# Performance work log

Measured on AMD Instinct MI355X. Metric: run time of the kernel, lower is better.

## Reference

```python
import jax, jax.numpy as jnp
import numpy as np

R = 4          # num_roles
L = 2          # num_layers
DIN = 128      # input/hidden feature dim
DOUT = 40     # output classes
N = 40000      # nodes
E = 480000     # edges


def setup_inputs() -> dict:
    key = jax.random.key(0)
    ks = jax.random.split(key, 12)
    x = jax.random.normal(ks[0], (N, R + DIN), dtype=jnp.float32)
    edge_index = jax.random.randint(ks[1], (2, E), 0, N, dtype=jnp.int64)
    s = 0.05
    Wm = jax.random.normal(ks[2], (L, R, DIN, DIN), dtype=jnp.float32) * s
    bm = jax.random.normal(ks[3], (L, R, DIN), dtype=jnp.float32) * s
    Wa = jax.random.normal(ks[4], (L, R, 2 * DIN, DIN), dtype=jnp.float32) * s
    ba = jax.random.normal(ks[5], (L, R, DIN), dtype=jnp.float32) * s
    W1 = jax.random.normal(ks[6], (DIN, DIN), dtype=jnp.float32) * s
    b1 = jax.random.normal(ks[7], (DIN,), dtype=jnp.float32) * s
    W2 = jax.random.normal(ks[8], (DIN, DOUT), dtype=jnp.float32) * s
    b2 = jax.random.normal(ks[9], (DOUT,), dtype=jnp.float32) * s
    return {"x": x, "edge_index": edge_index, "Wm": Wm, "bm": bm,
            "Wa": Wa, "ba": ba, "W1": W1, "b1": b1, "W2": W2, "b2": b2}


def _role_coef(roles):
    # Faithful to the original loop bug: linears[0] applied twice with roles[:,0],
    # linears[r] with roles[:,r] for r=1..R-2, linears[R-1] unused.
    return jnp.concatenate(
        [2.0 * roles[:, :1], roles[:, 1:R - 1], jnp.zeros_like(roles[:, :1])], axis=1)


def _graphsage_layer(xfull, src, dst, Wm_l, bm_l, Wa_l, ba_l):
    roles = xfull[:, :R]          # [N, R]
    feats = xfull[:, R:]          # [N, D]
    # --- message: gather source nodes, per-role linear + weighted sum, relu ---
    xr = roles[src]               # [E, R]
    xf = feats[src]               # [E, D]
    coef = _role_coef(xr)         # [E, R]
    lin = jnp.einsum('ei,rio->ero', xf, Wm_l) + bm_l[None]   # [E, R, O]
    msg = jax.nn.relu(jnp.einsum('er,ero->eo', coef, lin))    # [E, O]
    # --- aggregate: scatter-mean to target nodes ---
    ssum = jax.ops.segment_sum(msg, dst, num_segments=N)      # [N, O]
    cnt = jax.ops.segment_sum(jnp.ones((msg.shape[0], 1), msg.dtype), dst,
                              num_segments=N)                 # [N, 1]
    aggr = jnp.where(cnt > 0, ssum / jnp.maximum(cnt, 1.0), 0.0)
    # --- update: concat, per-role linear + weighted sum, relu, L2 normalize ---
    cat = jnp.concatenate([feats, aggr], axis=1)              # [N, D+O]
    coefn = _role_coef(roles)                                 # [N, R]
    lin2 = jnp.einsum('ni,rio->nro', cat, Wa_l) + ba_l[None]  # [N, R, O]
    out = jax.nn.relu(jnp.einsum('nr,nro->no', coefn, lin2))  # [N, O]
    norm = jnp.linalg.norm(out, axis=1, keepdims=True)
    return out / jnp.maximum(norm, 1e-12)


def reference(x, edge_index, Wm, bm, Wa, ba, W1, b1, W2, b2):
    src = edge_index[0]
    dst = edge_index[1]
    h = x
    for l in range(L):
        feats = _graphsage_layer(h, src, dst, Wm[l], bm[l], Wa[l], ba[l])
        feats = jax.nn.relu(feats)  # extra relu from GNNStack (dropout is identity in eval)
        h = jnp.concatenate([h[:, :R], feats], axis=1)
    z = h[:, R:]
    z = z @ W1 + b1               # post_mp linear 1 (dropout identity)
    logits = z @ W2 + b2          # post_mp linear 2
    return jax.nn.log_softmax(logits, axis=1)
```

## Files before the change

### kernel.cpp

```cpp
#include <hip/hip_runtime.h>
#include <hip/hip_fp16.h>

#define RN 4
#define XSTRIDE 132

typedef float    frag_cd __attribute__((ext_vector_type(4)));
typedef _Float16 frag_h  __attribute__((ext_vector_type(8)));

#define CW_M  (6 * 128 * 128)
#define CW_A  (6 * 128 * 256)
#define CW_1  (128 * 128)
#define CW_2  (48 * 128)
#define CW_TOT (CW_M + CW_A + CW_1 + CW_2)

__global__ void prep_kernel(
    const float* __restrict__ Wm, const float* __restrict__ Wa,
    const float* __restrict__ W1, const float* __restrict__ W2,
    _Float16* __restrict__ WmT, _Float16* __restrict__ WaT,
    _Float16* __restrict__ W1T, _Float16* __restrict__ W2T,
    const float* __restrict__ x, _Float16* __restrict__ X,
    const int* __restrict__ ei, int* __restrict__ cnt, int N, int E)
{
    int id = blockIdx.x * 256 + threadIdx.x;
    if (id < CW_M) {
        const int K = 128;
        int per = K * 128;
        int lr = id / per;  int l = lr / 3, r = lr - l * 3;
        int rem = id - lr * per;
        int k = rem >> 7, col = rem & 127;
        WmT[((size_t)lr * 128 + col) * K + k] =
            (_Float16)Wm[(((size_t)l * 4 + r) * K + k) * 128 + col];
        return;
    }
    id -= CW_M;
    if (id < CW_A) {
        const int K = 256;
        int per = K * 128;
        int lr = id / per;  int l = lr / 3, r = lr - l * 3;
        int rem = id - lr * per;
        int k = rem >> 7, col = rem & 127;
        WaT[((size_t)lr * 128 + col) * K + k] =
            (_Float16)Wa[(((size_t)l * 4 + r) * K + k) * 128 + col];
        return;
    }
    id -= CW_A;
    if (id < CW_1) {
        int col = id >> 7, k = id & 127;
        W1T[id] = (_Float16)W1[k * 128 + col];
        return;
    }
    id -= CW_1;
    if (id < CW_2) {
        int col = id >> 7, k = id & 127;
        W2T[id] = (_Float16)((col < 40) ? W2[k * 40 + col] : 0.0f);
        return;
    }
    id -= CW_2;
    if (id < N * 16) {
        int n = id >> 4, g = id & 15;
        const float4* src = (const float4*)(x + (size_t)n * XSTRIDE + RN + g * 8);
        float4 f0 = src[0], f1 = src[1];
        __half2 h0 = __float22half2_rn(make_float2(f0.x, f0.y));
        __half2 h1 = __float22half2_rn(make_float2(f0.z, f0.w));
        __half2 h2 = __float22half2_rn(make_float2(f1.x, f1.y));
        __half2 h3 = __float22half2_rn(make_float2(f1.z, f1.w));
        uint4 st; st.x = *(uint*)&h0; st.y = *(uint*)&h1;
        st.z = *(uint*)&h2; st.w = *(uint*)&h3;
        ((uint4*)X)[(size_t)n * 16 + g] = st;
        return;
    }
    id -= N * 16;
    if (id < E) atomicAdd(&cnt[ei[E + id]], 1);
}

__global__ void scanA(const int* __restrict__ cnt, int N, int* __restrict__ bsums) {
    __shared__ int s[256];
    int t = threadIdx.x, n = blockIdx.x * 256 + t;
    s[t] = (n < N) ? cnt[n] : 0;
    __syncthreads();
    for (int off = 128; off > 0; off >>= 1) {
        if (t < off) s[t] += s[t + off];
        __syncthreads();
    }
    if (t == 0) bsums[blockIdx.x] = s[0];
}

__global__ void scanC(const int* __restrict__ cnt, int N, int nb,
                      const int* __restrict__ bsums, int* __restrict__ offs) {
    __shared__ int s[256];
    __shared__ int basebuf[256];
    int t = threadIdx.x, n = blockIdx.x * 256 + t;
    int bid = blockIdx.x;
    basebuf[t] = (t < bid && t < nb) ? bsums[t] : 0;
    __syncthreads();
    for (int off = 128; off > 0; off >>= 1) {
        if (t < off) basebuf[t] += basebuf[t + off];
        __syncthreads();
    }
    int base = basebuf[0];
    int v = (n < N) ? cnt[n] : 0;
    s[t] = v; __syncthreads();
    for (int off = 1; off < 256; off <<= 1) {
        int add = (t >= off) ? s[t - off] : 0;
        __syncthreads();
        s[t] += add;
        __syncthreads();
    }
    if (n < N) {
        offs[n] = base + s[t] - v;
        if (n == N - 1) offs[N] = base + s[t];
    }
}

__global__ void fill_kernel(const int* __restrict__ ei, int E,
                            const int* __restrict__ offs, int* __restrict__ fc,
                            int* __restrict__ csr) {
    int e = blockIdx.x * 256 + threadIdx.x;
    if (e < E) {
        int dst = ei[E + e];
        int p = offs[dst] + atomicAdd(&fc[dst], 1);
        csr[p] = ei[e];
    }
}

__global__ __launch_bounds__(256) void agg_kernel(
    const int* __restrict__ csr, const int* __restrict__ offs,
    const _Float16* __restrict__ Mb, _Float16* __restrict__ S, int N)
{
    int node = blockIdx.x * 16 + (threadIdx.x >> 4);
    int lane = threadIdx.x & 15;
    if (node >= N) return;
    int lo = offs[node], hi = offs[node + 1];
    const uint4* M4 = (const uint4*)Mb;
    float a[8];
    #pragma unroll
    for (int i = 0; i < 8; ++i) a[i] = 0.0f;
    int e = lo;
    for (; e + 3 < hi; e += 4) {
        #pragma unroll
        for (int j = 0; j < 4; ++j) {
            uint4 u = M4[(size_t)csr[e + j] * 16 + lane];
            float2 f0 = __half22float2(*(const __half2*)&u.x);
            float2 f1 = __half22float2(*(const __half2*)&u.y);
            float2 f2 = __half22float2(*(const __half2*)&u.z);
            float2 f3 = __half22float2(*(const __half2*)&u.w);
            a[0] += f0.x; a[1] += f0.y; a[2] += f1.x; a[3] += f1.y;
            a[4] += f2.x; a[5] += f2.y; a[6] += f3.x; a[7] += f3.y;
        }
    }
    for (; e < hi; ++e) {
        uint4 u = M4[(size_t)csr[e] * 16 + lane];
        float2 f0 = __half22float2(*(const __half2*)&u.x);
        float2 f1 = __half22float2(*(const __half2*)&u.y);
        float2 f2 = __half22float2(*(const __half2*)&u.z);
        float2 f3 = __half22float2(*(const __half2*)&u.w);
        a[0] += f0.x; a[1] += f0.y; a[2] += f1.x; a[3] += f1.y;
        a[4] += f2.x; a[5] += f2.y; a[6] += f3.x; a[7] += f3.y;
    }
    float inv = (hi > lo) ? 1.0f / (float)(hi - lo) : 0.0f;
    __half2 h0 = __float22half2_rn(make_float2(a[0] * inv, a[1] * inv));
    __half2 h1 = __float22half2_rn(make_float2(a[2] * inv, a[3] * inv));
    __half2 h2 = __float22half2_rn(make_float2(a[4] * inv, a[5] * inv));
    __half2 h3 = __float22half2_rn(make_float2(a[6] * inv, a[7] * inv));
    uint4 st; st.x = *(uint*)&h0; st.y = *(uint*)&h1;
    st.z = *(uint*)&h2; st.w = *(uint*)&h3;
    ((uint4*)S)[(size_t)node * 16 + lane] = st;
}

#define STAGE_TILE(dst, src, n0, tid)                                         \
    _Pragma("unroll")                                                         \
    for (int i_ = 0; i_ < 4; ++i_) {                                          \
        int idx_ = i_ * 256 + (tid);                                          \
        int row_ = idx_ >> 4, g_ = idx_ & 15;                                 \
        *(uint4*)&(dst)[row_][g_ * 8] =                                       \
            ((const uint4*)(src))[((size_t)((n0) + row_)) * 16 + g_];         \
    }

__global__ __launch_bounds__(256) void msg_kernel(
    const float* __restrict__ x,
    const _Float16* __restrict__ Fp,
    const _Float16* __restrict__ W,
    const float* __restrict__ bias,
    _Float16* __restrict__ out)
{
    __shared__ _Float16 As[64][136];
    __shared__ float cc[64][3];

    const int tid = threadIdx.x;
    const int n0 = blockIdx.x * 64;
    const int lane = tid & 63;
    const int wv = tid >> 6;
    const int q = lane >> 4;
    const int lb = lane & 15;
    const int w32 = wv * 32;

    if (tid < 64) {
        const float* xr = x + (size_t)(n0 + tid) * XSTRIDE;
        cc[tid][0] = 2.0f * xr[0];
        cc[tid][1] = xr[1];
        cc[tid][2] = xr[2];
    }
    STAGE_TILE(As, Fp, n0, tid)
    __syncthreads();

    _Float16 ch16[4][3];
    #pragma unroll
    for (int nt = 0; nt < 4; ++nt)
        #pragma unroll
        for (int r = 0; r < 3; ++r)
            ch16[nt][r] = (_Float16)cc[nt * 16 + lb][r];

    frag_cd acc[4][2];
    #pragma unroll
    for (int nt = 0; nt < 4; ++nt)
        #pragma unroll
        for (int ct = 0; ct < 2; ++ct)
            acc[nt][ct] = (frag_cd){0.f, 0.f, 0.f, 0.f};

    frag_h bF[4][6];
    #pragma unroll
    for (int c = 0; c < 4; ++c)
        #pragma unroll
        for (int r = 0; r < 3; ++r)
            #pragma unroll
            for (int ct = 0; ct < 2; ++ct)
                bF[c][r * 2 + ct] = *(const frag_h*)(
                    W + ((size_t)(r * 128 + w32 + ct * 16 + lb)) * 128 + c * 32 + q * 8);

    frag_h aL[2][4];
    #pragma unroll
    for (int nt = 0; nt < 4; ++nt)
        aL[0][nt] = *(const frag_h*)&As[nt * 16 + lb][q * 8];

    #pragma unroll
    for (int c = 0; c < 4; ++c) {
        if (c + 1 < 4) {
            #pragma unroll
            for (int nt = 0; nt < 4; ++nt)
                aL[(c + 1) & 1][nt] = *(const frag_h*)&As[nt * 16 + lb][(c + 1) * 32 + q * 8];
        }
        #pragma unroll
        for (int r = 0; r < 3; ++r)
            #pragma unroll
            for (int nt = 0; nt < 4; ++nt) {
                frag_h sa = aL[c & 1][nt] * ch16[nt][r];
                #pragma unroll
                for (int ct = 0; ct < 2; ++ct)
                    acc[nt][ct] = __builtin_amdgcn_mfma_f32_16x16x32_f16(
                        sa, bF[c][r * 2 + ct], acc[nt][ct], 0, 0, 0);
            }
    }

    #pragma unroll
    for (int ct = 0; ct < 2; ++ct) {
        int col = w32 + ct * 16 + lb;
        float b0 = bias[col], b1 = bias[128 + col], b2 = bias[256 + col];
        #pragma unroll
        for (int nt = 0; nt < 4; ++nt)
            #pragma unroll
            for (int rg = 0; rg < 4; ++rg) {
                int row = nt * 16 + q * 4 + rg;
                float v = acc[nt][ct][rg]
                        + cc[row][0] * b0 + cc[row][1] * b1 + cc[row][2] * b2;
                out[(size_t)(n0 + row) * 128 + col] = (_Float16)fmaxf(v, 0.0f);
            }
    }
}

#define UPDATE_PHASE_A_LDS(Wa_, ba_)                                          \
    _Float16 ch16[4][3];                                                      \
    _Pragma("unroll")                                                         \
    for (int nt = 0; nt < 4; ++nt)                                            \
        _Pragma("unroll")                                                     \
        for (int r = 0; r < 3; ++r)                                           \
            ch16[nt][r] = (_Float16)cc[nt * 16 + lb][r];                      \
    frag_cd acc[4][2];                                                        \
    _Pragma("unroll")                                                         \
    for (int nt = 0; nt < 4; ++nt)                                            \
        _Pragma("unroll")                                                     \
        for (int ct = 0; ct < 2; ++ct)                                        \
            acc[nt][ct] = (frag_cd){0.f, 0.f, 0.f, 0.f};                      \
    size_t wrow[3][2];                                                        \
    _Pragma("unroll")                                                         \
    for (int r = 0; r < 3; ++r)                                               \
        _Pragma("unroll")                                                     \
        for (int ct = 0; ct < 2; ++ct)                                        \
            wrow[r][ct] = ((size_t)(r * 128 + w32 + ct * 16 + lb)) * 256 + q * 8; \
    {                                                                         \
        frag_h bF[3][6];                                                      \
        auto loadB = [&](int c, int buf) {                                    \
            _Pragma("unroll")                                                 \
            for (int r = 0; r < 3; ++r)                                       \
                _Pragma("unroll")                                             \
                for (int ct = 0; ct < 2; ++ct)                                \
                    bF[buf][r * 2 + ct] = *(const frag_h*)((Wa_) + wrow[r][ct] + c * 32); \
        };                                                                    \
        loadB(0, 0);                                                          \
        loadB(1, 1);                                                          \
        frag_h aL[2][4];                                                      \
        _Pragma("unroll")                                                     \
        for (int nt = 0; nt < 4; ++nt)                                        \
            aL[0][nt] = *(const frag_h*)&As[nt * 16 + lb][q * 8];             \
        _Pragma("unroll")                                                     \
        for (int ch = 0; ch < 8; ++ch) {                                      \
            if (ch + 2 < 8) loadB(ch + 2, (ch + 2) % 3);                      \
            if (ch + 1 < 8) {                                                 \
                const int c1 = ch + 1;                                        \
                _Pragma("unroll")                                             \
                for (int nt = 0; nt < 4; ++nt)                                \
                    aL[c1 & 1][nt] = (c1 < 4)                                 \
                        ? *(const frag_h*)&As[nt * 16 + lb][c1 * 32 + q * 8]  \
                        : *(const frag_h*)&Ss[nt * 16 + lb][(c1 - 4) * 32 + q * 8]; \
            }                                                                 \
            const int cur = ch % 3;                                           \
            _Pragma("unroll")                                                 \
            for (int r = 0; r < 3; ++r)                                       \
                _Pragma("unroll")                                             \
                for (int nt = 0; nt < 4; ++nt) {                              \
                    frag_h sa = aL[ch & 1][nt] * ch16[nt][r];                 \
                    _Pragma("unroll")                                         \
                    for (int ct = 0; ct < 2; ++ct)                            \
                        acc[nt][ct] = __builtin_amdgcn_mfma_f32_16x16x32_f16( \
                            sa, bF[cur][r * 2 + ct], acc[nt][ct], 0, 0, 0);   \
                }                                                             \
        }                                                                     \
    }                                                                         \
    float vv[4][2][4];                                                        \
    _Pragma("unroll")                                                         \
    for (int ct = 0; ct < 2; ++ct) {                                          \
        int col = w32 + ct * 16 + lb;                                         \
        float b0 = (ba_)[col], b1 = (ba_)[128 + col], b2 = (ba_)[256 + col];  \
        _Pragma("unroll")                                                     \
        for (int nt = 0; nt < 4; ++nt)                                        \
            _Pragma("unroll")                                                 \
            for (int rg = 0; rg < 4; ++rg) {                                  \
                int row = nt * 16 + q * 4 + rg;                               \
                float v = acc[nt][ct][rg]                                     \
                        + cc[row][0] * b0 + cc[row][1] * b1 + cc[row][2] * b2;\
                vv[nt][ct][rg] = fmaxf(v, 0.0f);                              \
            }                                                                 \
    }                                                                         \
    _Pragma("unroll")                                                         \
    for (int nt = 0; nt < 4; ++nt)                                            \
        _Pragma("unroll")                                                     \
        for (int rg = 0; rg < 4; ++rg) {                                      \
            float ss = vv[nt][0][rg] * vv[nt][0][rg] + vv[nt][1][rg] * vv[nt][1][rg]; \
            _Pragma("unroll")                                                 \
            for (int m = 1; m < 16; m <<= 1) ss += __shfl_xor(ss, m, 64);     \
            if (lb == 0) red[nt * 16 + q * 4 + rg][wv] = ss;                  \
        }                                                                     \
    __syncthreads();        \
    _Pragma("unroll")                                                         \
    for (int nt = 0; nt < 4; ++nt)                                            \
        _Pragma("unroll")                                                     \
        for (int rg = 0; rg < 4; ++rg) {                                      \
            int row = nt * 16 + q * 4 + rg;                                   \
            float t = red[row][0] + red[row][1] + red[row][2] + red[row][3];  \
            float inv = 1.0f / fmaxf(sqrtf(t), 1e-12f);                       \
            _Pragma("unroll")                                                 \
            for (int ct = 0; ct < 2; ++ct)                                    \
                Fs[row][w32 + ct * 16 + lb] = (_Float16)(vv[nt][ct][rg] * inv); \
        }                                                                     \
    __syncthreads();

__global__ __launch_bounds__(256) void fused_upd_msg(
    const float* __restrict__ x,
    const _Float16* __restrict__ Fp, const _Float16* __restrict__ Sp,
    const _Float16* __restrict__ Wa_, const float* __restrict__ ba_,
    const _Float16* __restrict__ Wm2, const float* __restrict__ bm2,
    _Float16* __restrict__ F1, _Float16* __restrict__ Mb)
{
    __shared__ _Float16 ldsbuf[2 * 64 * 136];
    __shared__ float cc[64][3];
    __shared__ float red[64][4];
    _Float16 (*As)[136] = (_Float16(*)[136])ldsbuf;
    _Float16 (*Ss)[136] = (_Float16(*)[136])(ldsbuf + 64 * 136);
    _Float16 (*Fs)[136] = As;

    const int tid = threadIdx.x;
    const int n0 = blockIdx.x * 64;
    const int lane = tid & 63;
    const int wv = tid >> 6;
    const int q = lane >> 4;
    const int lb = lane & 15;
    const int w32 = wv * 32;

    if (tid < 64) {
        const float* xr = x + (size_t)(n0 + tid) * XSTRIDE;
        cc[tid][0] = 2.0f * xr[0];
        cc[tid][1] = xr[1];
        cc[tid][2] = xr[2];
    }
    STAGE_TILE(As, Fp, n0, tid)
    STAGE_TILE(Ss, Sp, n0, tid)
    __syncthreads();

    UPDATE_PHASE_A_LDS(Wa_, ba_)

    #pragma unroll
    for (int i = 0; i < 4; ++i) {
        int idx = i * 256 + tid;
        int row = idx >> 4, g = idx & 15;
        ((uint4*)F1)[(size_t)(n0 + row) * 16 + g] = *(const uint4*)&Fs[row][g * 8];
    }

    frag_cd a2[4][2];
    #pragma unroll
    for (int nt = 0; nt < 4; ++nt)
        #pragma unroll
        for (int ct = 0; ct < 2; ++ct)
            a2[nt][ct] = (frag_cd){0.f, 0.f, 0.f, 0.f};

    frag_h bB[4][6];
    #pragma unroll
    for (int c = 0; c < 4; ++c)
        #pragma unroll
        for (int r = 0; r < 3; ++r)
            #pragma unroll
            for (int ct = 0; ct < 2; ++ct)
                bB[c][r * 2 + ct] = *(const frag_h*)(
                    Wm2 + ((size_t)(r * 128 + w32 + ct * 16 + lb)) * 128 + c * 32 + q * 8);

    #pragma unroll
    for (int c = 0; c < 4; ++c) {
        frag_h aM[4];
        #pragma unroll
        for (int nt = 0; nt < 4; ++nt)
            aM[nt] = *(const frag_h*)&Fs[nt * 16 + lb][c * 32 + q * 8];
        #pragma unroll
        for (int r = 0; r < 3; ++r)
            #pragma unroll
            for (int nt = 0; nt < 4; ++nt) {
                frag_h sa = aM[nt] * ch16[nt][r];
                #pragma unroll
                for (int ct = 0; ct < 2; ++ct)
                    a2[nt][ct] = __builtin_amdgcn_mfma_f32_16x16x32_f16(
                        sa, bB[c][r * 2 + ct], a2[nt][ct], 0, 0, 0);
            }
    }

    #pragma unroll
    for (int ct = 0; ct < 2; ++ct) {
        int col = w32 + ct * 16 + lb;
        float b0 = bm2[col], b1 = bm2[128 + col], b2 = bm2[256 + col];
        #pragma unroll
        for (int nt = 0; nt < 4; ++nt)
            #pragma unroll
            for (int rg = 0; rg < 4; ++rg) {
                int row = nt * 16 + q * 4 + rg;
                float v = a2[nt][ct][rg]
                        + cc[row][0] * b0 + cc[row][1] * b1 + cc[row][2] * b2;
                Mb[(size_t)(n0 + row) * 128 + col] = (_Float16)fmaxf(v, 0.0f);
            }
    }
}

__global__ __launch_bounds__(256) void fused_upd_final(
    const float* __restrict__ x,
    const _Float16* __restrict__ Fp, const _Float16* __restrict__ Sp,
    const _Float16* __restrict__ Wa_, const float* __restrict__ ba_,
    const _Float16* __restrict__ W1T, const float* __restrict__ b1,
    const _Float16* __restrict__ W2T, const float* __restrict__ b2,
    float* __restrict__ out)
{
    __shared__ _Float16 ldsbuf[2 * 64 * 136];
    __shared__ float cc[64][3];
    __shared__ float red[64][4];
    _Float16 (*As)[136] = (_Float16(*)[136])ldsbuf;
    _Float16 (*Ss)[136] = (_Float16(*)[136])(ldsbuf + 64 * 136);
    _Float16 (*Fs)[136] = As;
    _Float16 (*Z)[136]  = Ss;

    const int tid = threadIdx.x;
    const int n0 = blockIdx.x * 64;
    const int lane = tid & 63;
    const int wv = tid >> 6;
    const int q = lane >> 4;
    const int lb = lane & 15;
    const int w32 = wv * 32;

    if (tid < 64) {
        const float* xr = x + (size_t)(n0 + tid) * XSTRIDE;
        cc[tid][0] = 2.0f * xr[0];
        cc[tid][1] = xr[1];
        cc[tid][2] = xr[2];
    }
    STAGE_TILE(As, Fp, n0, tid)
    STAGE_TILE(Ss, Sp, n0, tid)
    __syncthreads();

    UPDATE_PHASE_A_LDS(Wa_, ba_)

    frag_cd az[4][2];
    #pragma unroll
    for (int nt = 0; nt < 4; ++nt)
        #pragma unroll
        for (int ct = 0; ct < 2; ++ct)
            az[nt][ct] = (frag_cd){0.f, 0.f, 0.f, 0.f};

    frag_h bZ[4][2];
    #pragma unroll
    for (int c = 0; c < 4; ++c)
        #pragma unroll
        for (int ct = 0; ct < 2; ++ct)
            bZ[c][ct] = *(const frag_h*)(
                W1T + (size_t)(w32 + ct * 16 + lb) * 128 + c * 32 + q * 8);

    #pragma unroll
    for (int c = 0; c < 4; ++c) {
        frag_h aZ[4];
        #pragma unroll
        for (int nt = 0; nt < 4; ++nt)
            aZ[nt] = *(const frag_h*)&Fs[nt * 16 + lb][c * 32 + q * 8];
        #pragma unroll
        for (int ct = 0; ct < 2; ++ct)
            #pragma unroll
            for (int nt = 0; nt < 4; ++nt)
                az[nt][ct] = __builtin_amdgcn_mfma_f32_16x16x32_f16(
                    aZ[nt], bZ[c][ct], az[nt][ct], 0, 0, 0);
    }
    __syncthreads();
    #pragma unroll
    for (int ct = 0; ct < 2; ++ct) {
        int col = w32 + ct * 16 + lb;
        float bb = b1[col];
        #pragma unroll
        for (int nt = 0; nt < 4; ++nt)
            #pragma unroll
            for (int rg = 0; rg < 4; ++rg)
                Z[nt * 16 + q * 4 + rg][col] = (_Float16)(az[nt][ct][rg] + bb);
    }
    __syncthreads();

    frag_cd a2[3];
    #pragma unroll
    for (int ct = 0; ct < 3; ++ct) a2[ct] = (frag_cd){0.f, 0.f, 0.f, 0.f};
    #pragma unroll
    for (int ch = 0; ch < 4; ++ch) {
        frag_h zF = *(const frag_h*)&Z[wv * 16 + lb][ch * 32 + q * 8];
        #pragma unroll
        for (int ct = 0; ct < 3; ++ct) {
            frag_h bF = *(const frag_h*)(W2T + (size_t)(ct * 16 + lb) * 128 + ch * 32 + q * 8);
            a2[ct] = __builtin_amdgcn_mfma_f32_16x16x32_f16(zF, bF, a2[ct], 0, 0, 0);
        }
    }

    float lg[3][4];
    #pragma unroll
    for (int ct = 0; ct < 3; ++ct) {
        int col = ct * 16 + lb;
        bool valid = col < 40;
        float bb = valid ? b2[col] : -1e30f;
        #pragma unroll
        for (int rg = 0; rg < 4; ++rg)
            lg[ct][rg] = valid ? (a2[ct][rg] + bb) : -1e30f;
    }
    #pragma unroll
    for (int rg = 0; rg < 4; ++rg) {
        float mx = fmaxf(fmaxf(lg[0][rg], lg[1][rg]), lg[2][rg]);
        #pragma unroll
        for (int m = 1; m < 16; m <<= 1) mx = fmaxf(mx, __shfl_xor(mx, m, 64));
        float sm = __expf(lg[0][rg] - mx) + __expf(lg[1][rg] - mx) + __expf(lg[2][rg] - mx);
        #pragma unroll
        for (int m = 1; m < 16; m <<= 1) sm += __shfl_xor(sm, m, 64);
        float ls = mx + __logf(sm);
        int row = n0 + wv * 16 + q * 4 + rg;
        #pragma unroll
        for (int ct = 0; ct < 3; ++ct) {
            int col = ct * 16 + lb;
            if (col < 40) out[(size_t)row * 40 + col] = lg[ct][rg] - ls;
        }
    }
}

extern "C" void kernel_launch(void* const* d_in, const int* in_sizes, int n_in,
                              void* d_out, int out_size, void* d_ws, size_t ws_size,
                              hipStream_t stream) {
    const float* x  = (const float*)d_in[0];
    const int*   ei = (const int*)d_in[1];
    const float* Wm = (const float*)d_in[2];
    const float* bm = (const float*)d_in[3];
    const float* Wa = (const float*)d_in[4];
    const float* ba = (const float*)d_in[5];
    const float* W1 = (const float*)d_in[6];
    const float* b1 = (const float*)d_in[7];
    const float* W2 = (const float*)d_in[8];
    const float* b2 = (const float*)d_in[9];
    float* out = (float*)d_out;

    const int N = in_sizes[0] / XSTRIDE;
    const int E = in_sizes[1] / 2;
    const int NB = (N + 255) / 256;
    const size_t P = (size_t)N * 128;

    _Float16* Mb  = (_Float16*)d_ws;
    _Float16* X   = Mb + P;
    _Float16* S   = X + P;
    _Float16* F1  = S + P;
    _Float16* WmT = F1 + P;
    _Float16* WaT = WmT + CW_M;
    _Float16* W1T = WaT + CW_A;
    _Float16* W2T = W1T + CW_1;
    int* cnt   = (int*)(W2T + CW_2);
    int* fc    = cnt + N;
    int* offs  = fc + N;
    int* csr   = offs + N + 1;
    int* bsums = csr + E;

    hipMemsetAsync(cnt, 0, (size_t)2 * N * sizeof(int), stream);
    const int prep_total = CW_TOT + N * 16 + E;
    prep_kernel<<<(prep_total + 255) / 256, 256, 0, stream>>>(
        Wm, Wa, W1, W2, WmT, WaT, W1T, W2T, x, X, ei, cnt, N, E);

    scanA<<<NB, 256, 0, stream>>>(cnt, N, bsums);
    scanC<<<NB, 256, 0, stream>>>(cnt, N, NB, bsums, offs);
    fill_kernel<<<(E + 255) / 256, 256, 0, stream>>>(ei, E, offs, fc, csr);

    const int gblk = N / 64;
    const int ablk = (N + 15) / 16;

    msg_kernel<<<gblk, 256, 0, stream>>>(x, X, WmT, bm, Mb);
    agg_kernel<<<ablk, 256, 0, stream>>>(csr, offs, Mb, S, N);
    fused_upd_msg<<<gblk, 256, 0, stream>>>(
        x, X, S, WaT, ba,
        WmT + (size_t)3 * 128 * 128, bm + (size_t)4 * 128, F1, Mb);
    agg_kernel<<<ablk, 256, 0, stream>>>(csr, offs, Mb, S, N);
    fused_upd_final<<<gblk, 256, 0, stream>>>(
        x, F1, S, WaT + (size_t)3 * 128 * 256, ba + (size_t)4 * 128,
        W1T, b1, W2T, b2, out);
}
```

Measured before the change: 266.1 us.

## Merge CSR fill into message kernel and preload all update weights

Folds the CSR fill work into the message GEMM launch as extra blocks, so both independent tasks run inside one dispatch and overlap. The update-kernel macro now loads all eight weight chunks into registers up front instead of keeping a three-stage rolling buffer. The fused update kernels also get a launch bound asking for two blocks per CU. The upfront loads raise register pressure, which combined with the occupancy hint could cause spills.

```diff
diff --git a/kernel.cpp b/kernel.cpp
--- a/kernel.cpp
+++ b/kernel.cpp
@@ -112,17 +112,6 @@
     }
 }
 
-__global__ void fill_kernel(const int* __restrict__ ei, int E,
-                            const int* __restrict__ offs, int* __restrict__ fc,
-                            int* __restrict__ csr) {
-    int e = blockIdx.x * 256 + threadIdx.x;
-    if (e < E) {
-        int dst = ei[E + e];
-        int p = offs[dst] + atomicAdd(&fc[dst], 1);
-        csr[p] = ei[e];
-    }
-}
-
 __global__ __launch_bounds__(256) void agg_kernel(
     const int* __restrict__ csr, const int* __restrict__ offs,
     const _Float16* __restrict__ Mb, _Float16* __restrict__ S, int N)
@@ -176,17 +165,30 @@
             ((const uint4*)(src))[((size_t)((n0) + row_)) * 16 + g_];         \
     }
 
-__global__ __launch_bounds__(256) void msg_kernel(
+__global__ __launch_bounds__(256) void msg_fill_kernel(
     const float* __restrict__ x,
     const _Float16* __restrict__ Fp,
     const _Float16* __restrict__ W,
     const float* __restrict__ bias,
-    _Float16* __restrict__ out)
+    _Float16* __restrict__ out,
+    const int* __restrict__ ei, int E,
+    const int* __restrict__ offs, int* __restrict__ fc,
+    int* __restrict__ csr, int msgB)
 {
     __shared__ _Float16 As[64][136];
     __shared__ float cc[64][3];
 
     const int tid = threadIdx.x;
+    if (blockIdx.x >= msgB) {
+        int e = (blockIdx.x - msgB) * 256 + tid;
+        if (e < E) {
+            int dst = ei[E + e];
+            int p = offs[dst] + atomicAdd(&fc[dst], 1);
+            csr[p] = ei[e];
+        }
+        return;
+    }
+
     const int n0 = blockIdx.x * 64;
     const int lane = tid & 63;
     const int wv = tid >> 6;
@@ -287,23 +289,20 @@
         for (int ct = 0; ct < 2; ++ct)                                        \
             wrow[r][ct] = ((size_t)(r * 128 + w32 + ct * 16 + lb)) * 256 + q * 8; \
     {                                                                         \
-        frag_h bF[3][6];                                                      \
-        auto loadB = [&](int c, int buf) {                                    \
+        frag_h bF[8][6];                                                      \
+        _Pragma("unroll")                                                     \
+        for (int c = 0; c < 8; ++c)                                           \
             _Pragma("unroll")                                                 \
             for (int r = 0; r < 3; ++r)                                       \
                 _Pragma("unroll")                                             \
                 for (int ct = 0; ct < 2; ++ct)                                \
-                    bF[buf][r * 2 + ct] = *(const frag_h*)((Wa_) + wrow[r][ct] + c * 32); \
-        };                                                                    \
-        loadB(0, 0);                                                          \
-        loadB(1, 1);                                                          \
+                    bF[c][r * 2 + ct] = *(const frag_h*)((Wa_) + wrow[r][ct] + c * 32); \
         frag_h aL[2][4];                                                      \
         _Pragma("unroll")                                                     \
         for (int nt = 0; nt < 4; ++nt)                                        \
             aL[0][nt] = *(const frag_h*)&As[nt * 16 + lb][q * 8];             \
         _Pragma("unroll")                                                     \
         for (int ch = 0; ch < 8; ++ch) {                                      \
-            if (ch + 2 < 8) loadB(ch + 2, (ch + 2) % 3);                      \
             if (ch + 1 < 8) {                                                 \
                 const int c1 = ch + 1;                                        \
                 _Pragma("unroll")                                             \
@@ -312,7 +311,6 @@
                         ? *(const frag_h*)&As[nt * 16 + lb][c1 * 32 + q * 8]  \
                         : *(const frag_h*)&Ss[nt * 16 + lb][(c1 - 4) * 32 + q * 8]; \
             }                                                                 \
-            const int cur = ch % 3;                                           \
             _Pragma("unroll")                                                 \
             for (int r = 0; r < 3; ++r)                                       \
                 _Pragma("unroll")                                             \
@@ -321,7 +319,7 @@
                     _Pragma("unroll")                                         \
                     for (int ct = 0; ct < 2; ++ct)                            \
                         acc[nt][ct] = __builtin_amdgcn_mfma_f32_16x16x32_f16( \
-                            sa, bF[cur][r * 2 + ct], acc[nt][ct], 0, 0, 0);   \
+                            sa, bF[ch][r * 2 + ct], acc[nt][ct], 0, 0, 0);    \
                 }                                                             \
         }                                                                     \
     }                                                                         \
@@ -349,7 +347,7 @@
             for (int m = 1; m < 16; m <<= 1) ss += __shfl_xor(ss, m, 64);     \
             if (lb == 0) red[nt * 16 + q * 4 + rg][wv] = ss;                  \
         }                                                                     \
-    __syncthreads();        \
+    __syncthreads();       \
     _Pragma("unroll")                                                         \
     for (int nt = 0; nt < 4; ++nt)                                            \
         _Pragma("unroll")                                                     \
@@ -363,7 +361,7 @@
         }                                                                     \
     __syncthreads();
 
-__global__ __launch_bounds__(256) void fused_upd_msg(
+__global__ __launch_bounds__(256, 2) void fused_upd_msg(
     const float* __restrict__ x,
     const _Float16* __restrict__ Fp, const _Float16* __restrict__ Sp,
     const _Float16* __restrict__ Wa_, const float* __restrict__ ba_,
@@ -455,7 +453,7 @@
     }
 }
 
-__global__ __launch_bounds__(256) void fused_upd_final(
+__global__ __launch_bounds__(256, 2) void fused_upd_final(
     const float* __restrict__ x,
     const _Float16* __restrict__ Fp, const _Float16* __restrict__ Sp,
     const _Float16* __restrict__ Wa_, const float* __restrict__ ba_,
@@ -614,12 +612,13 @@
 
     scanA<<<NB, 256, 0, stream>>>(cnt, N, bsums);
     scanC<<<NB, 256, 0, stream>>>(cnt, N, NB, bsums, offs);
-    fill_kernel<<<(E + 255) / 256, 256, 0, stream>>>(ei, E, offs, fc, csr);
 
     const int gblk = N / 64;
     const int ablk = (N + 15) / 16;
-
-    msg_kernel<<<gblk, 256, 0, stream>>>(x, X, WmT, bm, Mb);
+    const int fillB = (E + 255) / 256;
+
+    msg_fill_kernel<<<gblk + fillB, 256, 0, stream>>>(
+        x, X, WmT, bm, Mb, ei, E, offs, fc, csr, gblk);
     agg_kernel<<<ablk, 256, 0, stream>>>(csr, offs, Mb, S, N);
     fused_upd_msg<<<gblk, 256, 0, stream>>>(
         x, X, S, WaT, ba,
```

Result: faster. 254.2 us (-4.5%).
